# Kernel optimization log

Measured on AMD Instinct MI355X. Metric: run time of the kernel, lower is better.

Reference implementation:

```python
import jax, jax.numpy as jnp
import numpy as np

B, T, D, F, H, HID, OUT = 256, 512, 768, 1024, 8, 512, 256
EPS = 1e-5

def setup_inputs() -> dict:
    key = jax.random.key(0)
    ks = jax.random.split(key, 16)
    s = lambda fan_in: 1.0 / np.sqrt(fan_in)
    return {
        "x": jax.random.normal(ks[0], (B, F), jnp.float32),
        "text_feat": jax.random.normal(ks[1], (B, T, D), jnp.float32),
        "attention_mask": jax.random.randint(ks[2], (B, T), 0, 2, jnp.int32),
        # cross-attention params (torch Linear weight layout [out,in])
        "Wq": jax.random.normal(ks[3], (F, F), jnp.float32) * s(F),
        "bq": jnp.zeros((F,), jnp.float32),
        "Wk": jax.random.normal(ks[4], (F, D), jnp.float32) * s(D),
        "bk": jnp.zeros((F,), jnp.float32),
        "Wv": jax.random.normal(ks[5], (F, D), jnp.float32) * s(D),
        "bv": jnp.zeros((F,), jnp.float32),
        "Wo": jax.random.normal(ks[6], (F, F), jnp.float32) * s(F),
        "bo": jnp.zeros((F,), jnp.float32),
        # MLP: hidden Linear -> BatchNorm1d -> GELU, then output Linear
        "W1": jax.random.normal(ks[7], (HID, F), jnp.float32) * s(F),
        "b1": jnp.zeros((HID,), jnp.float32),
        "gamma": jnp.ones((HID,), jnp.float32),
        "beta": jnp.zeros((HID,), jnp.float32),
        "W2": jax.random.normal(ks[8], (OUT, HID), jnp.float32) * s(HID),
        "b2": jnp.zeros((OUT,), jnp.float32),
    }

def _forward(x, text_feat, attention_mask, Wq, bq, Wk, bk, Wv, bv, Wo, bo,
             W1, b1, gamma, beta, W2, b2):
    d = F // H
    q = (x @ Wq.T + bq).reshape(B, H, d)                      # [B,H,d] (q_len=1)
    k = (text_feat @ Wk.T + bk).reshape(B, T, H, d)           # [B,T,H,d]
    v = (text_feat @ Wv.T + bv).reshape(B, T, H, d)
    attn = jnp.einsum('bhd,bthd->bht', q, k) / jnp.sqrt(jnp.float32(d))
    attn = jnp.where(attention_mask[:, None, :] == 0, -jnp.inf, attn)
    attn = jax.nn.softmax(attn, axis=-1)                       # [B,H,T]
    out = jnp.einsum('bht,bthd->bhd', attn, v).reshape(B, F)
    out = out @ Wo.T + bo
    # MLP hidden: linear -> BatchNorm1d (training batch stats) -> GELU (exact)
    h = out @ W1.T + b1
    mu = jnp.mean(h, axis=0)
    var = jnp.var(h, axis=0)
    h = (h - mu) / jnp.sqrt(var + EPS) * gamma + beta
    h = jax.nn.gelu(h, approximate=False)
    return h @ W2.T + b2

def reference(x, text_feat, attention_mask, Wq, bq, Wk, bk, Wv, bv, Wo, bo,
              W1, b1, gamma, beta, W2, b2):
    return _forward(x, text_feat, attention_mask, Wq, bq, Wk, bk, Wv, bv, Wo, bo,
                    W1, b1, gamma, beta, W2, b2)
```

## Files before the change

kernel.cpp:

```cpp
#include <hip/hip_runtime.h>
#include <math.h>

#define Bb   256
#define Tt   512
#define Dd   768
#define Ff   1024
#define Hh   8
#define HIDh 512
#define OUTo 256

__device__ __forceinline__ void tr_tile(const float* __restrict__ in,
                                        float* __restrict__ out,
                                        int R, int C, int cx, int ry,
                                        float (*tile)[33])
{
    int c0 = cx * 32, r0 = ry * 32;
    int tx = threadIdx.x & 31, ty = threadIdx.x >> 5;
#pragma unroll
    for (int i = 0; i < 32; i += 8)
        tile[ty + i][tx] = in[(size_t)(r0 + ty + i) * C + c0 + tx];
    __syncthreads();
#pragma unroll
    for (int i = 0; i < 32; i += 8)
        out[(size_t)(c0 + ty + i) * R + r0 + tx] = tile[tx][ty + i];
}

__global__ __launch_bounds__(256) void prep(const float* __restrict__ Wq, float* __restrict__ WqT,
                                            const float* __restrict__ Wo, float* __restrict__ WoT,
                                            const float* __restrict__ Wv, float* __restrict__ WvT,
                                            const float* __restrict__ W1, float* __restrict__ W1T,
                                            const float* __restrict__ W2, float* __restrict__ W2T,
                                            const float* __restrict__ Wk, float* __restrict__ WkT)
{
    __shared__ float tile[32][33];
    int idx = blockIdx.x;
    if (idx < 1024) {
        tr_tile(Wq, WqT, 1024, 1024, idx & 31, idx >> 5, tile);
    } else if (idx < 2048) {
        int i2 = idx - 1024;
        tr_tile(Wo, WoT, 1024, 1024, i2 & 31, i2 >> 5, tile);
    } else if (idx < 2816) {
        int i2 = idx - 2048;
        tr_tile(Wv, WvT, 1024, 768, i2 % 24, i2 / 24, tile);
    } else if (idx < 3328) {
        int i2 = idx - 2816;
        tr_tile(W1, W1T, 512, 1024, i2 & 31, i2 >> 5, tile);
    } else if (idx < 3456) {
        int i2 = idx - 3328;
        tr_tile(W2, W2T, 256, 512, i2 & 15, i2 >> 4, tile);
    } else {
        int i2 = idx - 3456;
        int i = i2 >> 3, h = i2 & 7;
        for (int j = threadIdx.x; j < 768; j += 256)
            WkT[(size_t)(i * 8 + h) * 768 + j] = Wk[(size_t)(h * 128 + i) * 768 + j];
    }
}

#define FMA16(acc, a, w0, w1, w2, w3)                         \
    acc.x = fmaf(a.x, w0.x, acc.x); acc.y = fmaf(a.x, w0.y, acc.y); \
    acc.z = fmaf(a.x, w0.z, acc.z); acc.w = fmaf(a.x, w0.w, acc.w); \
    acc.x = fmaf(a.y, w1.x, acc.x); acc.y = fmaf(a.y, w1.y, acc.y); \
    acc.z = fmaf(a.y, w1.z, acc.z); acc.w = fmaf(a.y, w1.w, acc.w); \
    acc.x = fmaf(a.z, w2.x, acc.x); acc.y = fmaf(a.z, w2.y, acc.y); \
    acc.z = fmaf(a.z, w2.z, acc.z); acc.w = fmaf(a.z, w2.w, acc.w); \
    acc.x = fmaf(a.w, w3.x, acc.x); acc.y = fmaf(a.w, w3.y, acc.y); \
    acc.z = fmaf(a.w, w3.z, acc.z); acc.w = fmaf(a.w, w3.w, acc.w);

template<int CT, int RT, int R, int KS>
__global__ __launch_bounds__(256, 4) void gemm_sk(const float* __restrict__ A, int strideA,
                                                  const float* __restrict__ Wt, int N,
                                                  float* __restrict__ Cslab, int M)
{
    constexpr int CG = CT / 4;
    constexpr int RG = RT / R;
    static_assert(CG * RG == 256, "bad tile");
    const int cg = threadIdx.x % CG;
    const int rg = threadIdx.x / CG;
    const int cb = blockIdx.x, rb = blockIdx.y, ks = blockIdx.z;
    const int n0 = cb * CT + cg * 4;
    const int r0 = rb * RT;
    const int k0 = ks * KS;

    __shared__ float As[RT][KS + 4];
    for (int e = threadIdx.x * 4; e < RT * KS; e += 1024) {
        int r = e / KS, k = e % KS;
        *(float4*)&As[r][k] = *(const float4*)&A[(size_t)(r0 + r) * strideA + k0 + k];
    }
    __syncthreads();

    float4 acc[R];
#pragma unroll
    for (int rr = 0; rr < R; ++rr) acc[rr] = make_float4(0.f, 0.f, 0.f, 0.f);
    const float* wp = Wt + (size_t)k0 * N + n0;
#pragma unroll 2
    for (int k = 0; k < KS; k += 4) {
        float4 w0 = *(const float4*)&wp[(size_t)(k + 0) * N];
        float4 w1 = *(const float4*)&wp[(size_t)(k + 1) * N];
        float4 w2 = *(const float4*)&wp[(size_t)(k + 2) * N];
        float4 w3 = *(const float4*)&wp[(size_t)(k + 3) * N];
#pragma unroll
        for (int rr = 0; rr < R; ++rr) {
            float4 a = *(const float4*)&As[rg * R + rr][k];
            FMA16(acc[rr], a, w0, w1, w2, w3)
        }
    }
    float* cp = Cslab + (size_t)ks * M * N;
#pragma unroll
    for (int rr = 0; rr < R; ++rr)
        *(float4*)&cp[(size_t)(r0 + rg * R + rr) * N + n0] = acc[rr];
}

template<int CT, int RT, int R, int KS, int S>
__global__ __launch_bounds__(256, 4) void gemm_skf(const float* __restrict__ slabs,
                                                   size_t slabstride, int strideA,
                                                   const float* __restrict__ bias,
                                                   const float* __restrict__ Wt, int N,
                                                   float* __restrict__ Cslab, int M)
{
    constexpr int CG = CT / 4;
    constexpr int RG = RT / R;
    static_assert(CG * RG == 256, "bad tile");
    const int cg = threadIdx.x % CG;
    const int rg = threadIdx.x / CG;
    const int cb = blockIdx.x, rb = blockIdx.y, ks = blockIdx.z;
    const int n0 = cb * CT + cg * 4;
    const int r0 = rb * RT;
    const int k0 = ks * KS;

    __shared__ float As[RT][KS + 4];
    for (int e = threadIdx.x * 4; e < RT * KS; e += 1024) {
        int r = e / KS, k = e % KS;
        float4 acc = *(const float4*)&bias[k0 + k];
#pragma unroll
        for (int s = 0; s < S; ++s) {
            float4 v = *(const float4*)&slabs[(size_t)s * slabstride + (size_t)(r0 + r) * strideA + k0 + k];
            acc.x += v.x; acc.y += v.y; acc.z += v.z; acc.w += v.w;
        }
        *(float4*)&As[r][k] = acc;
    }
    __syncthreads();

    float4 acc[R];
#pragma unroll
    for (int rr = 0; rr < R; ++rr) acc[rr] = make_float4(0.f, 0.f, 0.f, 0.f);
    const float* wp = Wt + (size_t)k0 * N + n0;
#pragma unroll 2
    for (int k = 0; k < KS; k += 4) {
        float4 w0 = *(const float4*)&wp[(size_t)(k + 0) * N];
        float4 w1 = *(const float4*)&wp[(size_t)(k + 1) * N];
        float4 w2 = *(const float4*)&wp[(size_t)(k + 2) * N];
        float4 w3 = *(const float4*)&wp[(size_t)(k + 3) * N];
#pragma unroll
        for (int rr = 0; rr < R; ++rr) {
            float4 a = *(const float4*)&As[rg * R + rr][k];
            FMA16(acc[rr], a, w0, w1, w2, w3)
        }
    }
    float* cp = Cslab + (size_t)ks * M * N;
#pragma unroll
    for (int rr = 0; rr < R; ++rr)
        *(float4*)&cp[(size_t)(r0 + rg * R + rr) * N + n0] = acc[rr];
}

__global__ __launch_bounds__(256, 4) void qk_gemm(const float* __restrict__ qslab,
                                                  const float* __restrict__ bq,
                                                  const float* __restrict__ WkT,
                                                  float* __restrict__ qkfull)
{
    const int cg = threadIdx.x & 15;
    const int rg = threadIdx.x >> 4;
    const int cb = blockIdx.x, rb = blockIdx.y;
    const int n0 = cb * 64 + cg * 4;
    const int r0 = rb * 16;
    const int aoff = ((cb * 64) / 768) * 128;

    __shared__ float As[16][132];
    for (int e = threadIdx.x * 4; e < 16 * 128; e += 1024) {
        int r = e >> 7, k = e & 127;
        float4 acc = *(const float4*)&bq[aoff + k];
#pragma unroll
        for (int s = 0; s < 8; ++s) {
            float4 v = *(const float4*)&qslab[(size_t)s * 262144 + (size_t)(r0 + r) * 1024 + aoff + k];
            acc.x += v.x; acc.y += v.y; acc.z += v.z; acc.w += v.w;
        }
        *(float4*)&As[r][k] = acc;
    }
    __syncthreads();

    float4 acc = make_float4(0.f, 0.f, 0.f, 0.f);
    const float* wp = WkT + n0;
#pragma unroll 4
    for (int k = 0; k < 128; k += 4) {
        float4 w0 = *(const float4*)&wp[(size_t)(k + 0) * 6144];
        float4 w1 = *(const float4*)&wp[(size_t)(k + 1) * 6144];
        float4 w2 = *(const float4*)&wp[(size_t)(k + 2) * 6144];
        float4 w3 = *(const float4*)&wp[(size_t)(k + 3) * 6144];
        float4 a = *(const float4*)&As[rg][k];
        FMA16(acc, a, w0, w1, w2, w3)
    }
    *(float4*)&qkfull[(size_t)(r0 + rg) * 6144 + n0] = acc;
}

__global__ __launch_bounds__(256, 2) void attn_part(const float* __restrict__ text,
                                                    const int* __restrict__ mask,
                                                    const float* __restrict__ qk,
                                                    float* __restrict__ pctx,
                                                    float* __restrict__ psum)
{
    const int bx   = blockIdx.x;
    const int b    = bx >> 2;
    const int qt   = bx & 3;
    const int tid  = threadIdx.x;
    const int wv   = tid >> 6;
    const int lane = tid & 63;

    __shared__ float qk_s[Hh][Dd];
    __shared__ float ctx_s[Hh][Dd];
    __shared__ float wsum_s[4][Hh];
    __shared__ int   list_s[128];
    __shared__ int   wcnt_s[2];

    const float* qkp = qk + (size_t)b * (Hh * Dd);
    float* qf = (float*)qk_s;
    float* cf = (float*)ctx_s;
    for (int e = tid * 4; e < Hh * Dd; e += 1024) {
        *(float4*)&qf[e] = *(const float4*)&qkp[e];
        *(float4*)&cf[e] = make_float4(0.f, 0.f, 0.f, 0.f);
    }

    int m = 0, pre = 0, t = 0;
    if (wv < 2) {
        t = qt * 128 + wv * 64 + lane;
        m = mask[(size_t)b * Tt + t];
        unsigned long long bal = __ballot(m != 0);
        pre = __popcll(bal & ((1ull << lane) - 1ull));
        if (lane == 0) wcnt_s[wv] = __popcll(bal);
    }
    __syncthreads();
    if (wv < 2 && m) {
        int base = wv ? wcnt_s[0] : 0;
        list_s[base + pre] = t;
    }
    __syncthreads();
    const int cnt = wcnt_s[0] + wcnt_s[1];

    float s[Hh] = {0.f, 0.f, 0.f, 0.f, 0.f, 0.f, 0.f, 0.f};
    float4 cr[Hh][3];
#pragma unroll
    for (int h = 0; h < Hh; ++h)
#pragma unroll
        for (int c = 0; c < 3; ++c) cr[h][c] = make_float4(0.f, 0.f, 0.f, 0.f);

    const float scale = 0.08838834764831845f;
    const float* tbase = text + (size_t)b * Tt * Dd;

    int e = wv;
    float4 xa0, xa1, xa2;
    if (e < cnt) {
        const float* tp = tbase + (size_t)list_s[e] * Dd + 4 * lane;
        xa0 = *(const float4*)(tp);
        xa1 = *(const float4*)(tp + 256);
        xa2 = *(const float4*)(tp + 512);
    }
    while (e < cnt) {
        int en = e + 4;
        float4 xb0 = xa0, xb1 = xa1, xb2 = xa2;
        if (en < cnt) {
            const float* tp = tbase + (size_t)list_s[en] * Dd + 4 * lane;
            xb0 = *(const float4*)(tp);
            xb1 = *(const float4*)(tp + 256);
            xb2 = *(const float4*)(tp + 512);
        }
        float p[Hh];
#pragma unroll
        for (int h = 0; h < Hh; ++h) {
            const float* qh = &qk_s[h][4 * lane];
            float4 a0 = *(const float4*)(qh);
            float4 a1 = *(const float4*)(qh + 256);
            float4 a2 = *(const float4*)(qh + 512);
            float acc;
            acc = a0.x * xa0.x;
            acc = fmaf(a0.y, xa0.y, acc);
            acc = fmaf(a0.z, xa0.z, acc);
            acc = fmaf(a0.w, xa0.w, acc);
            acc = fmaf(a1.x, xa1.x, acc);
            acc = fmaf(a1.y, xa1.y, acc);
            acc = fmaf(a1.z, xa1.z, acc);
            acc = fmaf(a1.w, xa1.w, acc);
            acc = fmaf(a2.x, xa2.x, acc);
            acc = fmaf(a2.y, xa2.y, acc);
            acc = fmaf(a2.z, xa2.z, acc);
            acc = fmaf(a2.w, xa2.w, acc);
            p[h] = acc;
        }
#pragma unroll
        for (int h = 0; h < Hh; ++h) {
            float v = p[h];
            v += __shfl_xor(v, 1);
            v += __shfl_xor(v, 2);
            v += __shfl_xor(v, 4);
            v += __shfl_xor(v, 8);
            v += __shfl_xor(v, 16);
            v += __shfl_xor(v, 32);
            float w = __expf(v * scale);
            s[h] += w;
            cr[h][0].x = fmaf(w, xa0.x, cr[h][0].x);
            cr[h][0].y = fmaf(w, xa0.y, cr[h][0].y);
            cr[h][0].z = fmaf(w, xa0.z, cr[h][0].z);
            cr[h][0].w = fmaf(w, xa0.w, cr[h][0].w);
            cr[h][1].x = fmaf(w, xa1.x, cr[h][1].x);
            cr[h][1].y = fmaf(w, xa1.y, cr[h][1].y);
            cr[h][1].z = fmaf(w, xa1.z, cr[h][1].z);
            cr[h][1].w = fmaf(w, xa1.w, cr[h][1].w);
            cr[h][2].x = fmaf(w, xa2.x, cr[h][2].x);
            cr[h][2].y = fmaf(w, xa2.y, cr[h][2].y);
            cr[h][2].z = fmaf(w, xa2.z, cr[h][2].z);
            cr[h][2].w = fmaf(w, xa2.w, cr[h][2].w);
        }
        xa0 = xb0; xa1 = xb1; xa2 = xb2;
        e = en;
    }

    if (lane == 0) {
#pragma unroll
        for (int h = 0; h < Hh; ++h) wsum_s[wv][h] = s[h];
    }

    for (int w4 = 0; w4 < 4; ++w4) {
        __syncthreads();
        if (wv == w4) {
#pragma unroll
            for (int h = 0; h < Hh; ++h) {
                float* cp = &ctx_s[h][4 * lane];
#pragma unroll
                for (int c = 0; c < 3; ++c) {
                    float4 cur = *(float4*)(cp + c * 256);
                    cur.x += cr[h][c].x;
                    cur.y += cr[h][c].y;
                    cur.z += cr[h][c].z;
                    cur.w += cr[h][c].w;
                    *(float4*)(cp + c * 256) = cur;
                }
            }
        }
    }
    __syncthreads();

    if (tid < Hh) {
        float S = wsum_s[0][tid] + wsum_s[1][tid] + wsum_s[2][tid] + wsum_s[3][tid];
        psum[(size_t)bx * Hh + tid] = S;
    }
    float* outp = pctx + (size_t)bx * (Hh * Dd);
    for (int e2 = tid * 4; e2 < Hh * Dd; e2 += 1024)
        *(float4*)&outp[e2] = *(const float4*)&cf[e2];
}

__global__ __launch_bounds__(256, 4) void v_gemm(const float* __restrict__ pctx,
                                                 const float* __restrict__ psum,
                                                 const float* __restrict__ WvT,
                                                 float* __restrict__ aoslab)
{
    const int cg = threadIdx.x & 31;
    const int rg = threadIdx.x >> 5;
    const int h = blockIdx.x, rb = blockIdx.y, ks = blockIdx.z;
    const int n0 = h * 128 + cg * 4;
    const int r0 = rb * 32;
    const int k0 = ks * 128;

    __shared__ float As[32][132];
    __shared__ float sv[32];

    if (threadIdx.x < 32) {
        int row = r0 + threadIdx.x;
        float S = 0.f;
#pragma unroll
        for (int i = 0; i < 4; ++i) S += psum[(size_t)(row * 4 + i) * Hh + h];
        sv[threadIdx.x] = 1.0f / S;
    }
    __syncthreads();
    for (int e = threadIdx.x * 4; e < 32 * 128; e += 1024) {
        int r = e >> 7, k = e & 127;
        size_t col = (size_t)h * 768 + k0 + k;
        float4 acc = make_float4(0.f, 0.f, 0.f, 0.f);
#pragma unroll
        for (int i = 0; i < 4; ++i) {
            float4 v = *(const float4*)&pctx[((size_t)(r0 + r) * 4 + i) * 6144 + col];
            acc.x += v.x; acc.y += v.y; acc.z += v.z; acc.w += v.w;
        }
        float svv = sv[r];
        acc.x *= svv; acc.y *= svv; acc.z *= svv; acc.w *= svv;
        *(float4*)&As[r][k] = acc;
    }
    __syncthreads();

    float4 acc[4];
#pragma unroll
    for (int rr = 0; rr < 4; ++rr) acc[rr] = make_float4(0.f, 0.f, 0.f, 0.f);
    const float* wp = WvT + (size_t)k0 * 1024 + n0;
#pragma unroll 2
    for (int k = 0; k < 128; k += 4) {
        float4 w0 = *(const float4*)&wp[(size_t)(k + 0) * 1024];
        float4 w1 = *(const float4*)&wp[(size_t)(k + 1) * 1024];
        float4 w2 = *(const float4*)&wp[(size_t)(k + 2) * 1024];
        float4 w3 = *(const float4*)&wp[(size_t)(k + 3) * 1024];
#pragma unroll
        for (int rr = 0; rr < 4; ++rr) {
            float4 a = *(const float4*)&As[rg * 4 + rr][k];
            FMA16(acc[rr], a, w0, w1, w2, w3)
        }
    }
    float* cp = aoslab + (size_t)ks * 262144;
#pragma unroll
    for (int rr = 0; rr < 4; ++rr)
        *(float4*)&cp[(size_t)(r0 + rg * 4 + rr) * 1024 + n0] = acc[rr];
}

__global__ __launch_bounds__(256) void bn_stats2(const float* __restrict__ h1slab,
                                                 const float* __restrict__ b1,
                                                 const float* __restrict__ gamma,
                                                 const float* __restrict__ beta,
                                                 float* __restrict__ scl,
                                                 float* __restrict__ shf)
{
    int c8 = threadIdx.x & 7, rg = threadIdx.x >> 3;
    int c = blockIdx.x * 8 + c8;
    float bias = b1[c];
    float sum = 0.f, sq = 0.f;
    for (int r = rg; r < Bb; r += 32) {
        float v = bias;
#pragma unroll
        for (int s = 0; s < 8; ++s)
            v += h1slab[(size_t)s * 131072 + (size_t)r * HIDh + c];
        sum += v;
        sq = fmaf(v, v, sq);
    }
    __shared__ float ss[32][8], sq_[32][8];
    ss[rg][c8] = sum; sq_[rg][c8] = sq;
    for (int off = 16; off > 0; off >>= 1) {
        __syncthreads();
        if (rg < off) { ss[rg][c8] += ss[rg + off][c8]; sq_[rg][c8] += sq_[rg + off][c8]; }
    }
    __syncthreads();
    if (rg == 0) {
        float mu  = ss[0][c8] * (1.0f / Bb);
        float var = sq_[0][c8] * (1.0f / Bb) - mu * mu;
        float g   = gamma[c] * rsqrtf(var + 1e-5f);
        scl[c] = g;
        shf[c] = fmaf(-mu, g, beta[c]);
    }
}

__global__ __launch_bounds__(256, 4) void gelu2(const float* __restrict__ h1slab,
                                                const float* __restrict__ b1,
                                                const float* __restrict__ scl,
                                                const float* __restrict__ shf,
                                                const float* __restrict__ W2T,
                                                const float* __restrict__ b2,
                                                float* __restrict__ out)
{
    const int cg = threadIdx.x & 15;
    const int rg = threadIdx.x >> 4;
    const int n0 = blockIdx.x * 64 + cg * 4;
    const int r0 = blockIdx.y * 16;

    __shared__ float As[16][132];
    float4 acc = make_float4(0.f, 0.f, 0.f, 0.f);

    for (int k0 = 0; k0 < HIDh; k0 += 128) {
        __syncthreads();
        for (int e = threadIdx.x * 4; e < 2048; e += 1024) {
            int r = e >> 7, k = e & 127;
            float4 v = *(const float4*)&b1[k0 + k];
#pragma unroll
            for (int s = 0; s < 8; ++s) {
                float4 u = *(const float4*)&h1slab[(size_t)s * 131072 + (size_t)(r0 + r) * HIDh + k0 + k];
                v.x += u.x; v.y += u.y; v.z += u.z; v.w += u.w;
            }
            float4 sc = *(const float4*)&scl[k0 + k];
            float4 sh = *(const float4*)&shf[k0 + k];
            float4 z;
            z.x = fmaf(v.x, sc.x, sh.x);
            z.y = fmaf(v.y, sc.y, sh.y);
            z.z = fmaf(v.z, sc.z, sh.z);
            z.w = fmaf(v.w, sc.w, sh.w);
            z.x = 0.5f * z.x * (1.0f + erff(z.x * 0.70710678118654752f));
            z.y = 0.5f * z.y * (1.0f + erff(z.y * 0.70710678118654752f));
            z.z = 0.5f * z.z * (1.0f + erff(z.z * 0.70710678118654752f));
            z.w = 0.5f * z.w * (1.0f + erff(z.w * 0.70710678118654752f));
            *(float4*)&As[r][k] = z;
        }
        __syncthreads();
        const float* wp = W2T + (size_t)k0 * OUTo + n0;
#pragma unroll 2
        for (int k = 0; k < 128; k += 4) {
            float4 w0 = *(const float4*)&wp[(size_t)(k + 0) * OUTo];
            float4 w1 = *(const float4*)&wp[(size_t)(k + 1) * OUTo];
            float4 w2 = *(const float4*)&wp[(size_t)(k + 2) * OUTo];
            float4 w3 = *(const float4*)&wp[(size_t)(k + 3) * OUTo];
            float4 a = *(const float4*)&As[rg][k];
            FMA16(acc, a, w0, w1, w2, w3)
        }
    }

    float4 bvv = *(const float4*)&b2[n0];
    acc.x += bvv.x; acc.y += bvv.y; acc.z += bvv.z; acc.w += bvv.w;
    *(float4*)&out[(size_t)(r0 + rg) * OUTo + n0] = acc;
}

extern "C" void kernel_launch(void* const* d_in, const int* in_sizes, int n_in,
                              void* d_out, int out_size, void* d_ws, size_t ws_size,
                              hipStream_t stream)
{
    const float* x     = (const float*)d_in[0];
    const float* text  = (const float*)d_in[1];
    const int*   amask = (const int*)d_in[2];
    const float* Wq    = (const float*)d_in[3];
    const float* bq    = (const float*)d_in[4];
    const float* Wk    = (const float*)d_in[5];
    const float* Wv    = (const float*)d_in[7];
    const float* bv    = (const float*)d_in[8];
    const float* Wo    = (const float*)d_in[9];
    const float* bo    = (const float*)d_in[10];
    const float* W1    = (const float*)d_in[11];
    const float* b1    = (const float*)d_in[12];
    const float* gamma = (const float*)d_in[13];
    const float* beta  = (const float*)d_in[14];
    const float* W2    = (const float*)d_in[15];
    const float* b2    = (const float*)d_in[16];

    float* ws     = (float*)d_ws;
    float* WqT    = ws;
    float* WoT    = WqT    + 1048576;
    float* WkT    = WoT    + 1048576;
    float* WvT    = WkT    + 786432;
    float* W1T    = WvT    + 786432;
    float* W2T    = W1T    + 524288;
    float* qslab  = W2T    + 131072;
    float* qkfull = qslab  + 2097152;
    float* pctx   = qkfull + 1572864;
    float* psum   = pctx   + 6291456;
    float* aoslab = psum   + 8192;
    float* oslab  = aoslab + 1572864;
    float* h1slab = oslab  + 2097152;
    float* scl    = h1slab + 1048576;
    float* shf    = scl    + 512;

    prep<<<4480, 256, 0, stream>>>(Wq, WqT, Wo, WoT, Wv, WvT, W1, W1T, W2, W2T, Wk, WkT);

    gemm_sk<128, 32, 4, 128><<<dim3(8, 8, 8), 256, 0, stream>>>(x, 1024, WqT, 1024, qslab, 256);

    qk_gemm<<<dim3(96, 16), 256, 0, stream>>>(qslab, bq, WkT, qkfull);

    attn_part<<<1024, 256, 0, stream>>>(text, amask, qkfull, pctx, psum);

    v_gemm<<<dim3(8, 8, 6), 256, 0, stream>>>(pctx, psum, WvT, aoslab);

    gemm_skf<128, 32, 4, 128, 6><<<dim3(8, 8, 8), 256, 0, stream>>>(aoslab, 262144, 1024, bv, WoT, 1024, oslab, 256);

    gemm_skf<64, 32, 2, 128, 8><<<dim3(8, 8, 8), 256, 0, stream>>>(oslab, 262144, 1024, bo, W1T, 512, h1slab, 256);

    bn_stats2<<<64, 256, 0, stream>>>(h1slab, b1, gamma, beta, scl, shf);

    gelu2<<<dim3(4, 16), 256, 0, stream>>>(h1slab, b1, scl, shf, W2T, b2, (float*)d_out);
}
```

Measured before the change: 251.9 us.

## Restructure attention into one block per batch with LDS double-buffered text tiles

Replaces the four-way split attention kernel (1024 blocks of 256 threads writing partial contexts and sums) with one 512-thread block per batch row. Each block stages eight unmasked text rows at a time in shared memory with register-prefetch double buffering, and each wave handles four heads whose query vectors stay in registers. The softmax normalization moves into the attention kernel, so v_gemm reads a single normalized context instead of summing four partial slabs, which cuts the partial-context write and reread traffic. It also vectorizes the weight transposes with float4 accesses. The trade-off is only 256 blocks at one block per CU with heavy LDS use, which may leave the GPU underoccupied.

```diff
diff --git a/kernel.cpp b/kernel.cpp
--- a/kernel.cpp
+++ b/kernel.cpp
@@ -9,20 +9,26 @@
 #define HIDh 512
 #define OUTo 256
 
-__device__ __forceinline__ void tr_tile(const float* __restrict__ in,
-                                        float* __restrict__ out,
-                                        int R, int C, int cx, int ry,
-                                        float (*tile)[33])
+__device__ __forceinline__ void tr_tile4(const float* __restrict__ in,
+                                         float* __restrict__ out,
+                                         int R, int C, int cx, int ry,
+                                         float (*tile)[33])
 {
     int c0 = cx * 32, r0 = ry * 32;
-    int tx = threadIdx.x & 31, ty = threadIdx.x >> 5;
-#pragma unroll
-    for (int i = 0; i < 32; i += 8)
-        tile[ty + i][tx] = in[(size_t)(r0 + ty + i) * C + c0 + tx];
-    __syncthreads();
-#pragma unroll
-    for (int i = 0; i < 32; i += 8)
-        out[(size_t)(c0 + ty + i) * R + r0 + tx] = tile[tx][ty + i];
+    int r  = threadIdx.x >> 3;
+    int c4 = (threadIdx.x & 7) * 4;
+    float4 v = *(const float4*)&in[(size_t)(r0 + r) * C + c0 + c4];
+    tile[r][c4 + 0] = v.x;
+    tile[r][c4 + 1] = v.y;
+    tile[r][c4 + 2] = v.z;
+    tile[r][c4 + 3] = v.w;
+    __syncthreads();
+    float4 o;
+    o.x = tile[c4 + 0][r];
+    o.y = tile[c4 + 1][r];
+    o.z = tile[c4 + 2][r];
+    o.w = tile[c4 + 3][r];
+    *(float4*)&out[(size_t)(c0 + r) * R + r0 + c4] = o;
 }
 
 __global__ __launch_bounds__(256) void prep(const float* __restrict__ Wq, float* __restrict__ WqT,
@@ -35,24 +41,27 @@
     __shared__ float tile[32][33];
     int idx = blockIdx.x;
     if (idx < 1024) {
-        tr_tile(Wq, WqT, 1024, 1024, idx & 31, idx >> 5, tile);
+        tr_tile4(Wq, WqT, 1024, 1024, idx & 31, idx >> 5, tile);
     } else if (idx < 2048) {
         int i2 = idx - 1024;
-        tr_tile(Wo, WoT, 1024, 1024, i2 & 31, i2 >> 5, tile);
+        tr_tile4(Wo, WoT, 1024, 1024, i2 & 31, i2 >> 5, tile);
     } else if (idx < 2816) {
         int i2 = idx - 2048;
-        tr_tile(Wv, WvT, 1024, 768, i2 % 24, i2 / 24, tile);
+        tr_tile4(Wv, WvT, 1024, 768, i2 % 24, i2 / 24, tile);
     } else if (idx < 3328) {
         int i2 = idx - 2816;
-        tr_tile(W1, W1T, 512, 1024, i2 & 31, i2 >> 5, tile);
+        tr_tile4(W1, W1T, 512, 1024, i2 & 31, i2 >> 5, tile);
     } else if (idx < 3456) {
         int i2 = idx - 3328;
-        tr_tile(W2, W2T, 256, 512, i2 & 15, i2 >> 4, tile);
+        tr_tile4(W2, W2T, 256, 512, i2 & 15, i2 >> 4, tile);
     } else {
         int i2 = idx - 3456;
         int i = i2 >> 3, h = i2 & 7;
-        for (int j = threadIdx.x; j < 768; j += 256)
-            WkT[(size_t)(i * 8 + h) * 768 + j] = Wk[(size_t)(h * 128 + i) * 768 + j];
+        if (threadIdx.x < 192) {
+            int j = threadIdx.x * 4;
+            *(float4*)&WkT[(size_t)(i * 8 + h) * 768 + j] =
+                *(const float4*)&Wk[(size_t)(h * 128 + i) * 768 + j];
+        }
     }
 }
 
@@ -76,10 +85,9 @@
     static_assert(CG * RG == 256, "bad tile");
     const int cg = threadIdx.x % CG;
     const int rg = threadIdx.x / CG;
-    const int cb = blockIdx.x, rb = blockIdx.y, ks = blockIdx.z;
-    const int n0 = cb * CT + cg * 4;
-    const int r0 = rb * RT;
-    const int k0 = ks * KS;
+    const int n0 = blockIdx.x * CT + cg * 4;
+    const int r0 = blockIdx.y * RT;
+    const int k0 = blockIdx.z * KS;
 
     __shared__ float As[RT][KS + 4];
     for (int e = threadIdx.x * 4; e < RT * KS; e += 1024) {
@@ -104,7 +112,7 @@
             FMA16(acc[rr], a, w0, w1, w2, w3)
         }
     }
-    float* cp = Cslab + (size_t)ks * M * N;
+    float* cp = Cslab + (size_t)blockIdx.z * M * N;
 #pragma unroll
     for (int rr = 0; rr < R; ++rr)
         *(float4*)&cp[(size_t)(r0 + rg * R + rr) * N + n0] = acc[rr];
@@ -122,10 +130,9 @@
     static_assert(CG * RG == 256, "bad tile");
     const int cg = threadIdx.x % CG;
     const int rg = threadIdx.x / CG;
-    const int cb = blockIdx.x, rb = blockIdx.y, ks = blockIdx.z;
-    const int n0 = cb * CT + cg * 4;
-    const int r0 = rb * RT;
-    const int k0 = ks * KS;
+    const int n0 = blockIdx.x * CT + cg * 4;
+    const int r0 = blockIdx.y * RT;
+    const int k0 = blockIdx.z * KS;
 
     __shared__ float As[RT][KS + 4];
     for (int e = threadIdx.x * 4; e < RT * KS; e += 1024) {
@@ -156,7 +163,7 @@
             FMA16(acc[rr], a, w0, w1, w2, w3)
         }
     }
-    float* cp = Cslab + (size_t)ks * M * N;
+    float* cp = Cslab + (size_t)blockIdx.z * M * N;
 #pragma unroll
     for (int rr = 0; rr < R; ++rr)
         *(float4*)&cp[(size_t)(r0 + rg * R + rr) * N + n0] = acc[rr];
@@ -201,162 +208,202 @@
     *(float4*)&qkfull[(size_t)(r0 + rg) * 6144 + n0] = acc;
 }
 
-__global__ __launch_bounds__(256, 2) void attn_part(const float* __restrict__ text,
+__device__ __forceinline__ float dot12(float4 a0, float4 a1, float4 a2,
+                                       float4 x0, float4 x1, float4 x2)
+{
+    float acc;
+    acc = a0.x * x0.x;
+    acc = fmaf(a0.y, x0.y, acc);
+    acc = fmaf(a0.z, x0.z, acc);
+    acc = fmaf(a0.w, x0.w, acc);
+    acc = fmaf(a1.x, x1.x, acc);
+    acc = fmaf(a1.y, x1.y, acc);
+    acc = fmaf(a1.z, x1.z, acc);
+    acc = fmaf(a1.w, x1.w, acc);
+    acc = fmaf(a2.x, x2.x, acc);
+    acc = fmaf(a2.y, x2.y, acc);
+    acc = fmaf(a2.z, x2.z, acc);
+    acc = fmaf(a2.w, x2.w, acc);
+    return acc;
+}
+
+__global__ __launch_bounds__(512, 1) void attn_ctx2(const float* __restrict__ text,
                                                     const int* __restrict__ mask,
                                                     const float* __restrict__ qk,
-                                                    float* __restrict__ pctx,
-                                                    float* __restrict__ psum)
-{
-    const int bx   = blockIdx.x;
-    const int b    = bx >> 2;
-    const int qt   = bx & 3;
-    const int tid  = threadIdx.x;
-    const int wv   = tid >> 6;
-    const int lane = tid & 63;
-
-    __shared__ float qk_s[Hh][Dd];
+                                                    float* __restrict__ ctx)
+{
+    const int b     = blockIdx.x;
+    const int tid   = threadIdx.x;
+    const int wv    = tid >> 6;
+    const int lane  = tid & 63;
+    const int hbase = wv & 4;
+    const int rsel  = wv & 3;
+
     __shared__ float ctx_s[Hh][Dd];
-    __shared__ float wsum_s[4][Hh];
-    __shared__ int   list_s[128];
-    __shared__ int   wcnt_s[2];
+    __shared__ float tbuf[2][8][Dd];
+    __shared__ float wsum_s[8][4];
+    __shared__ float sinv_s[Hh];
+    __shared__ int   list_s[Tt];
+    __shared__ int   wcnt_s[8];
 
     const float* qkp = qk + (size_t)b * (Hh * Dd);
-    float* qf = (float*)qk_s;
+    float4 qkr[4][3];
+#pragma unroll
+    for (int hh = 0; hh < 4; ++hh)
+#pragma unroll
+        for (int c = 0; c < 3; ++c)
+            qkr[hh][c] = *(const float4*)&qkp[(hbase + hh) * Dd + c * 256 + 4 * lane];
+
     float* cf = (float*)ctx_s;
-    for (int e = tid * 4; e < Hh * Dd; e += 1024) {
-        *(float4*)&qf[e] = *(const float4*)&qkp[e];
+    for (int e = tid * 4; e < Hh * Dd; e += 2048)
         *(float4*)&cf[e] = make_float4(0.f, 0.f, 0.f, 0.f);
-    }
-
-    int m = 0, pre = 0, t = 0;
-    if (wv < 2) {
-        t = qt * 128 + wv * 64 + lane;
-        m = mask[(size_t)b * Tt + t];
+
+    {
+        int t = wv * 64 + lane;
+        int m = mask[(size_t)b * Tt + t];
         unsigned long long bal = __ballot(m != 0);
-        pre = __popcll(bal & ((1ull << lane) - 1ull));
+        int pre = __popcll(bal & ((1ull << lane) - 1ull));
         if (lane == 0) wcnt_s[wv] = __popcll(bal);
-    }
-    __syncthreads();
-    if (wv < 2 && m) {
-        int base = wv ? wcnt_s[0] : 0;
-        list_s[base + pre] = t;
-    }
-    __syncthreads();
-    const int cnt = wcnt_s[0] + wcnt_s[1];
-
-    float s[Hh] = {0.f, 0.f, 0.f, 0.f, 0.f, 0.f, 0.f, 0.f};
-    float4 cr[Hh][3];
-#pragma unroll
-    for (int h = 0; h < Hh; ++h)
-#pragma unroll
-        for (int c = 0; c < 3; ++c) cr[h][c] = make_float4(0.f, 0.f, 0.f, 0.f);
-
+        __syncthreads();
+        if (m) {
+            int base = 0;
+            for (int w = 0; w < wv; ++w) base += wcnt_s[w];
+            list_s[base + pre] = t;
+        }
+        __syncthreads();
+    }
+    int cnt = 0;
+#pragma unroll
+    for (int w = 0; w < 8; ++w) cnt += wcnt_s[w];
+    const int nb = (cnt + 7) >> 3;
+
+    const float* tbase = text + (size_t)b * (size_t)(Tt * Dd);
+
+    const int sr0 = tid / 192,           sc0 = (tid % 192) * 4;
+    const int sr1 = (tid + 512) / 192,   sc1 = ((tid + 512) % 192) * 4;
+    const int sr2 = (tid + 1024) / 192,  sc2 = ((tid + 1024) % 192) * 4;
+
+#define ISSUE(dst, bi)                                                           \
+    {                                                                            \
+        int ri0 = (bi) * 8 + sr0, ri1 = (bi) * 8 + sr1, ri2 = (bi) * 8 + sr2;    \
+        if (ri0 < cnt) dst[0] = *(const float4*)&tbase[(size_t)list_s[ri0] * Dd + sc0]; \
+        if (ri1 < cnt) dst[1] = *(const float4*)&tbase[(size_t)list_s[ri1] * Dd + sc1]; \
+        if (ri2 < cnt) dst[2] = *(const float4*)&tbase[(size_t)list_s[ri2] * Dd + sc2]; \
+    }
+#define COMMIT(src, buf)                                                         \
+    {                                                                            \
+        *(float4*)&tbuf[buf][sr0][sc0] = src[0];                                 \
+        *(float4*)&tbuf[buf][sr1][sc1] = src[1];                                 \
+        *(float4*)&tbuf[buf][sr2][sc2] = src[2];                                 \
+    }
+
+    float4 ldA[3], ldB[3];
+    ldA[0] = ldA[1] = ldA[2] = make_float4(0.f, 0.f, 0.f, 0.f);
+    ldB[0] = ldB[1] = ldB[2] = ldA[0];
+
+    ISSUE(ldA, 0)
+    COMMIT(ldA, 0)
+    if (nb > 1) ISSUE(ldA, 1)
+    __syncthreads();
+
+    float4 cr[4][3];
+#pragma unroll
+    for (int hh = 0; hh < 4; ++hh)
+#pragma unroll
+        for (int c = 0; c < 3; ++c) cr[hh][c] = make_float4(0.f, 0.f, 0.f, 0.f);
+    float s[4] = {0.f, 0.f, 0.f, 0.f};
     const float scale = 0.08838834764831845f;
-    const float* tbase = text + (size_t)b * Tt * Dd;
-
-    int e = wv;
-    float4 xa0, xa1, xa2;
-    if (e < cnt) {
-        const float* tp = tbase + (size_t)list_s[e] * Dd + 4 * lane;
-        xa0 = *(const float4*)(tp);
-        xa1 = *(const float4*)(tp + 256);
-        xa2 = *(const float4*)(tp + 512);
-    }
-    while (e < cnt) {
-        int en = e + 4;
-        float4 xb0 = xa0, xb1 = xa1, xb2 = xa2;
-        if (en < cnt) {
-            const float* tp = tbase + (size_t)list_s[en] * Dd + 4 * lane;
-            xb0 = *(const float4*)(tp);
-            xb1 = *(const float4*)(tp + 256);
-            xb2 = *(const float4*)(tp + 512);
-        }
-        float p[Hh];
-#pragma unroll
-        for (int h = 0; h < Hh; ++h) {
-            const float* qh = &qk_s[h][4 * lane];
-            float4 a0 = *(const float4*)(qh);
-            float4 a1 = *(const float4*)(qh + 256);
-            float4 a2 = *(const float4*)(qh + 512);
-            float acc;
-            acc = a0.x * xa0.x;
-            acc = fmaf(a0.y, xa0.y, acc);
-            acc = fmaf(a0.z, xa0.z, acc);
-            acc = fmaf(a0.w, xa0.w, acc);
-            acc = fmaf(a1.x, xa1.x, acc);
-            acc = fmaf(a1.y, xa1.y, acc);
-            acc = fmaf(a1.z, xa1.z, acc);
-            acc = fmaf(a1.w, xa1.w, acc);
-            acc = fmaf(a2.x, xa2.x, acc);
-            acc = fmaf(a2.y, xa2.y, acc);
-            acc = fmaf(a2.z, xa2.z, acc);
-            acc = fmaf(a2.w, xa2.w, acc);
-            p[h] = acc;
-        }
-#pragma unroll
-        for (int h = 0; h < Hh; ++h) {
-            float v = p[h];
-            v += __shfl_xor(v, 1);
-            v += __shfl_xor(v, 2);
-            v += __shfl_xor(v, 4);
-            v += __shfl_xor(v, 8);
-            v += __shfl_xor(v, 16);
-            v += __shfl_xor(v, 32);
-            float w = __expf(v * scale);
-            s[h] += w;
-            cr[h][0].x = fmaf(w, xa0.x, cr[h][0].x);
-            cr[h][0].y = fmaf(w, xa0.y, cr[h][0].y);
-            cr[h][0].z = fmaf(w, xa0.z, cr[h][0].z);
-            cr[h][0].w = fmaf(w, xa0.w, cr[h][0].w);
-            cr[h][1].x = fmaf(w, xa1.x, cr[h][1].x);
-            cr[h][1].y = fmaf(w, xa1.y, cr[h][1].y);
-            cr[h][1].z = fmaf(w, xa1.z, cr[h][1].z);
-            cr[h][1].w = fmaf(w, xa1.w, cr[h][1].w);
-            cr[h][2].x = fmaf(w, xa2.x, cr[h][2].x);
-            cr[h][2].y = fmaf(w, xa2.y, cr[h][2].y);
-            cr[h][2].z = fmaf(w, xa2.z, cr[h][2].z);
-            cr[h][2].w = fmaf(w, xa2.w, cr[h][2].w);
-        }
-        xa0 = xb0; xa1 = xb1; xa2 = xb2;
-        e = en;
-    }
-
-    if (lane == 0) {
-#pragma unroll
-        for (int h = 0; h < Hh; ++h) wsum_s[wv][h] = s[h];
-    }
-
-    for (int w4 = 0; w4 < 4; ++w4) {
-        __syncthreads();
-        if (wv == w4) {
-#pragma unroll
-            for (int h = 0; h < Hh; ++h) {
-                float* cp = &ctx_s[h][4 * lane];
-#pragma unroll
-                for (int c = 0; c < 3; ++c) {
-                    float4 cur = *(float4*)(cp + c * 256);
-                    cur.x += cr[h][c].x;
-                    cur.y += cr[h][c].y;
-                    cur.z += cr[h][c].z;
-                    cur.w += cr[h][c].w;
-                    *(float4*)(cp + c * 256) = cur;
+
+    for (int i = 0; i < nb; ++i) {
+        const int cur = i & 1;
+        if (i + 2 < nb) {
+            if (cur == 0) { ISSUE(ldB, i + 2) } else { ISSUE(ldA, i + 2) }
+        }
+#pragma unroll
+        for (int rr = 0; rr < 2; ++rr) {
+            int r = rsel + rr * 4;
+            if (i * 8 + r < cnt) {
+                float4 x0 = *(const float4*)&tbuf[cur][r][4 * lane];
+                float4 x1 = *(const float4*)&tbuf[cur][r][256 + 4 * lane];
+                float4 x2 = *(const float4*)&tbuf[cur][r][512 + 4 * lane];
+                float px[4];
+#pragma unroll
+                for (int hh = 0; hh < 4; ++hh)
+                    px[hh] = dot12(qkr[hh][0], qkr[hh][1], qkr[hh][2], x0, x1, x2);
+#pragma unroll
+                for (int hh = 0; hh < 4; ++hh) {
+                    float v = px[hh];
+                    v += __shfl_xor(v, 1);
+                    v += __shfl_xor(v, 2);
+                    v += __shfl_xor(v, 4);
+                    v += __shfl_xor(v, 8);
+                    v += __shfl_xor(v, 16);
+                    v += __shfl_xor(v, 32);
+                    float w = __expf(v * scale);
+                    s[hh] += w;
+                    cr[hh][0].x = fmaf(w, x0.x, cr[hh][0].x);
+                    cr[hh][0].y = fmaf(w, x0.y, cr[hh][0].y);
+                    cr[hh][0].z = fmaf(w, x0.z, cr[hh][0].z);
+                    cr[hh][0].w = fmaf(w, x0.w, cr[hh][0].w);
+                    cr[hh][1].x = fmaf(w, x1.x, cr[hh][1].x);
+                    cr[hh][1].y = fmaf(w, x1.y, cr[hh][1].y);
+                    cr[hh][1].z = fmaf(w, x1.z, cr[hh][1].z);
+                    cr[hh][1].w = fmaf(w, x1.w, cr[hh][1].w);
+                    cr[hh][2].x = fmaf(w, x2.x, cr[hh][2].x);
+                    cr[hh][2].y = fmaf(w, x2.y, cr[hh][2].y);
+                    cr[hh][2].z = fmaf(w, x2.z, cr[hh][2].z);
+                    cr[hh][2].w = fmaf(w, x2.w, cr[hh][2].w);
                 }
             }
         }
+        if (i + 1 < nb) {
+            if (cur == 0) { COMMIT(ldA, 1) } else { COMMIT(ldB, 0) }
+        }
+        __syncthreads();
+    }
+#undef ISSUE
+#undef COMMIT
+
+    if (lane == 0) {
+#pragma unroll
+        for (int hh = 0; hh < 4; ++hh) wsum_s[wv][hh] = s[hh];
+    }
+
+    for (int rnd = 0; rnd < 4; ++rnd) {
+        __syncthreads();
+        int hh = (rsel + rnd) & 3;
+        float* cp = &ctx_s[hbase + hh][4 * lane];
+#pragma unroll
+        for (int c = 0; c < 3; ++c) {
+            float4 cu = *(float4*)(cp + c * 256);
+            cu.x += cr[hh][c].x;
+            cu.y += cr[hh][c].y;
+            cu.z += cr[hh][c].z;
+            cu.w += cr[hh][c].w;
+            *(float4*)(cp + c * 256) = cu;
+        }
     }
     __syncthreads();
 
     if (tid < Hh) {
-        float S = wsum_s[0][tid] + wsum_s[1][tid] + wsum_s[2][tid] + wsum_s[3][tid];
-        psum[(size_t)bx * Hh + tid] = S;
-    }
-    float* outp = pctx + (size_t)bx * (Hh * Dd);
-    for (int e2 = tid * 4; e2 < Hh * Dd; e2 += 1024)
-        *(float4*)&outp[e2] = *(const float4*)&cf[e2];
-}
-
-__global__ __launch_bounds__(256, 4) void v_gemm(const float* __restrict__ pctx,
-                                                 const float* __restrict__ psum,
+        int h = tid;
+        int wb = h & 4;
+        float S = wsum_s[wb + 0][h & 3] + wsum_s[wb + 1][h & 3] +
+                  wsum_s[wb + 2][h & 3] + wsum_s[wb + 3][h & 3];
+        sinv_s[h] = 1.0f / S;
+    }
+    __syncthreads();
+
+    float* outp = ctx + (size_t)b * (Hh * Dd);
+    for (int e = tid * 4; e < Hh * Dd; e += 2048) {
+        float4 v = *(const float4*)&cf[e];
+        float si = sinv_s[e / Dd];
+        v.x *= si; v.y *= si; v.z *= si; v.w *= si;
+        *(float4*)&outp[e] = v;
+    }
+}
+
+__global__ __launch_bounds__(256, 4) void v_gemm(const float* __restrict__ ctx,
                                                  const float* __restrict__ WvT,
                                                  float* __restrict__ aoslab)
 {
@@ -368,28 +415,9 @@
     const int k0 = ks * 128;
 
     __shared__ float As[32][132];
-    __shared__ float sv[32];
-
-    if (threadIdx.x < 32) {
-        int row = r0 + threadIdx.x;
-        float S = 0.f;
-#pragma unroll
-        for (int i = 0; i < 4; ++i) S += psum[(size_t)(row * 4 + i) * Hh + h];
-        sv[threadIdx.x] = 1.0f / S;
-    }
-    __syncthreads();
     for (int e = threadIdx.x * 4; e < 32 * 128; e += 1024) {
         int r = e >> 7, k = e & 127;
-        size_t col = (size_t)h * 768 + k0 + k;
-        float4 acc = make_float4(0.f, 0.f, 0.f, 0.f);
-#pragma unroll
-        for (int i = 0; i < 4; ++i) {
-            float4 v = *(const float4*)&pctx[((size_t)(r0 + r) * 4 + i) * 6144 + col];
-            acc.x += v.x; acc.y += v.y; acc.z += v.z; acc.w += v.w;
-        }
-        float svv = sv[r];
-        acc.x *= svv; acc.y *= svv; acc.z *= svv; acc.w *= svv;
-        *(float4*)&As[r][k] = acc;
+        *(float4*)&As[r][k] = *(const float4*)&ctx[(size_t)(r0 + r) * 6144 + (size_t)h * 768 + k0 + k];
     }
     __syncthreads();
 
@@ -537,9 +565,8 @@
     float* W2T    = W1T    + 524288;
     float* qslab  = W2T    + 131072;
     float* qkfull = qslab  + 2097152;
-    float* pctx   = qkfull + 1572864;
-    float* psum   = pctx   + 6291456;
-    float* aoslab = psum   + 8192;
+    float* ctx    = qkfull + 1572864;
+    float* aoslab = ctx    + 1572864;
     float* oslab  = aoslab + 1572864;
     float* h1slab = oslab  + 2097152;
     float* scl    = h1slab + 1048576;
@@ -551,9 +578,9 @@
 
     qk_gemm<<<dim3(96, 16), 256, 0, stream>>>(qslab, bq, WkT, qkfull);
 
-    attn_part<<<1024, 256, 0, stream>>>(text, amask, qkfull, pctx, psum);
-
-    v_gemm<<<dim3(8, 8, 6), 256, 0, stream>>>(pctx, psum, WvT, aoslab);
+    attn_ctx2<<<256, 512, 0, stream>>>(text, amask, qkfull, ctx);
+
+    v_gemm<<<dim3(8, 8, 6), 256, 0, stream>>>(ctx, WvT, aoslab);
 
     gemm_skf<128, 32, 4, 128, 6><<<dim3(8, 8, 8), 256, 0, stream>>>(aoslab, 262144, 1024, bv, WoT, 1024, oslab, 256);
 
```

Measured after the change: 471.5 us. 1.87x slower.
